# Performance work log

Hardware: AMD Instinct MI355X
Metric: run time of the kernel (lower is better)

The kernel has to match this reference:

```python
import jax, jax.numpy as jnp
import numpy as np

N, E, NG = 10000, 160000, 64
HID, HEADS = 256, 4
NEG_SLOPE = 0.2


def setup_inputs() -> dict:
    key = jax.random.key(0)
    ks = jax.random.split(key, 20)
    s = 0.1
    inp = {
        "atom_features": jax.random.normal(ks[0], (N, 23), jnp.float32),
        "edge_index": jax.random.randint(ks[1], (2, E), 0, N),
        "batch": jnp.sort(jax.random.randint(ks[2], (N,), 0, NG)),
        "W1": jax.random.normal(ks[3], (23, HEADS * HID), jnp.float32) * s,
        "as1": jax.random.normal(ks[4], (HEADS, HID), jnp.float32) * s,
        "ad1": jax.random.normal(ks[5], (HEADS, HID), jnp.float32) * s,
        "b1": jnp.zeros((HEADS * HID,), jnp.float32),
        "W2": jax.random.normal(ks[6], (HEADS * HID, HEADS * HID), jnp.float32) * s,
        "as2": jax.random.normal(ks[7], (HEADS, HID), jnp.float32) * s,
        "ad2": jax.random.normal(ks[8], (HEADS, HID), jnp.float32) * s,
        "b2": jnp.zeros((HEADS * HID,), jnp.float32),
        "W3": jax.random.normal(ks[9], (HEADS * HID, HID), jnp.float32) * s,
        "as3": jax.random.normal(ks[10], (1, HID), jnp.float32) * s,
        "ad3": jax.random.normal(ks[11], (1, HID), jnp.float32) * s,
        "b3": jnp.zeros((HID,), jnp.float32),
        # MLP head
        "fc1_w": jax.random.normal(ks[12], (HID, HID // 2), jnp.float32) * s,
        "fc1_b": jnp.zeros((HID // 2,), jnp.float32),
        "fc2_w": jax.random.normal(ks[13], (HID // 2, 1), jnp.float32) * s,
        "fc2_b": jnp.zeros((1,), jnp.float32),
    }
    return inp


def gat_layer(x, W, att_src, att_dst, bias, src, dst, heads, ch):
    n = x.shape[0]
    h = (x @ W).reshape(n, heads, ch)                      # [N,H,C]
    a_s = jnp.sum(h * att_src, axis=-1)                    # [N,H]
    a_d = jnp.sum(h * att_dst, axis=-1)                    # [N,H]
    logits = jax.nn.leaky_relu(a_s[src] + a_d[dst], NEG_SLOPE)  # [E',H]
    m = jax.ops.segment_max(logits, dst, num_segments=n)
    m = jnp.where(jnp.isfinite(m), m, 0.0)
    e = jnp.exp(logits - m[dst])
    denom = jax.ops.segment_sum(e, dst, num_segments=n)
    alpha = e / (denom[dst] + 1e-16)                       # segment softmax over incoming edges
    out = jax.ops.segment_sum(alpha[:, :, None] * h[src], dst, num_segments=n)
    return out.reshape(n, heads * ch) + bias


def reference(atom_features, edge_index, batch,
              W1, as1, ad1, b1, W2, as2, ad2, b2, W3, as3, ad3, b3,
              fc1_w, fc1_b, fc2_w, fc2_b):
    n = atom_features.shape[0]
    loops = jnp.arange(n)
    src = jnp.concatenate([edge_index[0], loops])   # PyG GATConv adds self-loops
    dst = jnp.concatenate([edge_index[1], loops])

    x = jax.nn.elu(gat_layer(atom_features, W1, as1, ad1, b1, src, dst, HEADS, HID))
    x = jax.nn.elu(gat_layer(x, W2, as2, ad2, b2, src, dst, HEADS, HID))
    x = jax.nn.elu(gat_layer(x, W3, as3, ad3, b3, src, dst, 1, HID))
    # dropout: eval mode (training=False) -> identity

    # global mean pool over molecules
    sums = jax.ops.segment_sum(x, batch, num_segments=NG)
    counts = jax.ops.segment_sum(jnp.ones((n,), x.dtype), batch, num_segments=NG)
    features = sums / jnp.maximum(counts, 1.0)[:, None]    # [NG, HID]

    hmid = jax.nn.relu(features @ fc1_w + fc1_b)
    validity = hmid @ fc2_w + fc2_b                        # [NG, 1]
    return validity, features
```

## Files before the change

### kernel.cpp

```cpp
#include <hip/hip_runtime.h>
#include <hip/hip_bf16.h>
#include <math.h>

typedef unsigned short ushortT;
typedef __attribute__((ext_vector_type(8))) short short8;
typedef __attribute__((ext_vector_type(4))) float f32x4;

constexpr int NN   = 10000;
constexpr int EE   = 160000;
constexpr int ETOT = EE + NN;
constexpr int NG   = 64;
constexpr int HID  = 256;
constexpr int HEADS = 4;

__device__ __forceinline__ ushortT f2bf(float x) {
    __hip_bfloat16 h = __float2bfloat16(x);
    return *reinterpret_cast<ushortT*>(&h);
}
__device__ __forceinline__ float bf2f(ushortT x) {
    unsigned u = ((unsigned)x) << 16;
    return __uint_as_float(u);
}

__device__ __forceinline__ int xcd_swz(int flat, int nwg) {
    int q = nwg >> 3, r = nwg & 7;
    int xcd = flat & 7, j = flat >> 3;
    return (xcd < r ? xcd * (q + 1) : r * (q + 1) + (xcd - r) * q) + j;
}

__global__ __launch_bounds__(256) void setup_kernel(
        const float* __restrict__ W1, const float* __restrict__ as1,
        const float* __restrict__ ad1, float* __restrict__ wsv1,
        const float* __restrict__ W2, const float* __restrict__ as2,
        const float* __restrict__ ad2, float* __restrict__ wsv2,
        const float* __restrict__ W3, const float* __restrict__ as3,
        const float* __restrict__ ad3, float* __restrict__ wsv3,
        ushortT* __restrict__ wt2, ushortT* __restrict__ wt3,
        ushortT* __restrict__ b1p, int* __restrict__ cnt) {
    __shared__ float t[32][33];
    const int b = blockIdx.x, tid = threadIdx.x;
    if (b < 1280) {
        const float* W; ushortT* Wt; int N, n0, k0;
        if (b < 1024) { W = W2; Wt = wt2; N = 1024; n0 = (b & 31) * 32; k0 = (b >> 5) * 32; }
        else          { int b2 = b - 1024; W = W3; Wt = wt3; N = 256; n0 = (b2 & 7) * 32; k0 = (b2 >> 3) * 32; }
        const int K = 1024, Kp = 1024;
        int tx = tid & 31, ty = tid >> 5;
        for (int i = ty; i < 32; i += 8) {
            int k = k0 + i, n = n0 + tx;
            t[i][tx] = (k < K && n < N) ? W[(size_t)k * N + n] : 0.f;
        }
        __syncthreads();
        for (int i = ty; i < 32; i += 8) {
            int n = n0 + i, kp = k0 + tx;
            if (n < N && kp < Kp) Wt[(size_t)n * Kp + kp] = f2bf(t[tx][i]);
        }
    } else if (b < 1792) {
        int idx = (b - 1280) * 256 + tid;
        int n = idx >> 7, kp = idx & 127;
        int h = n >> 8, hk = kp >> 5, k = kp & 31;
        float v = (hk == h && k < 23) ? W1[(size_t)k * 1024 + n] : 0.f;
        b1p[idx] = f2bf(v);
    } else if (b < 4398) {
        int gw = (b - 1792) * 4 + (tid >> 6);
        int lane = tid & 63;
        const float *W, *atts, *attd; float* wsv; int heads, idx;
        if (gw < 184)            { W = W1; atts = as1; attd = ad1; wsv = wsv1; heads = 4; idx = gw; }
        else if (gw < 184 + 8192){ W = W2; atts = as2; attd = ad2; wsv = wsv2; heads = 4; idx = gw - 184; }
        else if (gw < 184 + 8192 + 2048) { W = W3; atts = as3; attd = ad3; wsv = wsv3; heads = 1; idx = gw - 184 - 8192; }
        else return;
        const int nout = 2 * heads;
        int k = idx / nout, o = idx - k * nout;
        int h = (o >= heads) ? (o - heads) : o;
        const float* att  = ((o >= heads) ? attd : atts) + h * HID;
        const float* wrow = W + (size_t)k * (heads * HID) + h * HID;
        float4 w4 = *(const float4*)(wrow + lane * 4);
        float4 a4 = *(const float4*)(att + lane * 4);
        float s = w4.x * a4.x + w4.y * a4.y + w4.z * a4.z + w4.w * a4.w;
        #pragma unroll
        for (int off = 1; off < 64; off <<= 1) s += __shfl_xor(s, off);
        if (lane == 0) wsv[(size_t)k * nout + o] = s;
    } else {
        int idx = (b - 4398) * 256 + tid;
        if (idx < NN) cnt[idx] = 0;
    }
}

__global__ void edge_count_kernel(const int* __restrict__ ei, int* __restrict__ cnt) {
    int e = blockIdx.x * blockDim.x + threadIdx.x;
    if (e >= ETOT) return;
    int dst = (e < EE) ? ei[EE + e] : (e - EE);
    atomicAdd(&cnt[dst], 1);
}

__global__ void scan_kernel(const int* __restrict__ cnt, int* __restrict__ row_ptr,
                            int* __restrict__ cursor) {
    __shared__ int part[256];
    int tid = threadIdx.x;
    const int chunk = (NN + 255) / 256;
    int s0 = tid * chunk;
    int s1 = min(NN, s0 + chunk);
    int sum = 0;
    for (int i = s0; i < s1; ++i) sum += cnt[i];
    part[tid] = sum;
    __syncthreads();
    for (int off = 1; off < 256; off <<= 1) {
        int v = (tid >= off) ? part[tid - off] : 0;
        __syncthreads();
        part[tid] += v;
        __syncthreads();
    }
    int run = (tid == 0) ? 0 : part[tid - 1];
    for (int i = s0; i < s1; ++i) {
        row_ptr[i] = run;
        cursor[i]  = run;
        run += cnt[i];
    }
    if (tid == 255) row_ptr[NN] = part[255];
}

__global__ void fill_dots1_kernel(const int* __restrict__ ei, int* __restrict__ cursor,
                                  int* __restrict__ col_src,
                                  const float* __restrict__ atom,
                                  const float* __restrict__ wsv1,
                                  float* __restrict__ a_s, float* __restrict__ a_d,
                                  int nfill) {
    int b = blockIdx.x;
    if (b < nfill) {
        int e = b * 256 + threadIdx.x;
        if (e >= ETOT) return;
        int src, dst;
        if (e < EE) { src = ei[e]; dst = ei[EE + e]; }
        else        { src = dst = e - EE; }
        int pos = atomicAdd(&cursor[dst], 1);
        col_src[pos] = src;
    } else {
        int n = (b - nfill) * 256 + threadIdx.x;
        if (n >= NN) return;
        float a[8] = {0.f, 0.f, 0.f, 0.f, 0.f, 0.f, 0.f, 0.f};
        #pragma unroll
        for (int k = 0; k < 23; ++k) {
            float x = atom[n * 23 + k];
            #pragma unroll
            for (int o = 0; o < 8; ++o) a[o] += x * wsv1[k * 8 + o];
        }
        #pragma unroll
        for (int h = 0; h < 4; ++h) { a_s[n * 4 + h] = a[h]; a_d[n * 4 + h] = a[4 + h]; }
    }
}

__global__ __launch_bounds__(256) void agg_atom_kernel(const float* __restrict__ atom,
                                                       const float* __restrict__ a_s,
                                                       const float* __restrict__ a_d,
                                                       const int* __restrict__ rowp,
                                                       const int* __restrict__ colv,
                                                       ushortT* __restrict__ Ap) {
    const int wv = threadIdx.x >> 6, lane = threadIdx.x & 63;
    const int i = blockIdx.x * 4 + wv;
    if (i >= NN) return;
    const int half = lane >> 5, c = lane & 31;
    const int start = rowp[i], end = rowp[i + 1];

    __shared__ float wsh[4][64][4];
    __shared__ int   ssh[4][64];

    float acc[4] = {0.f, 0.f, 0.f, 0.f};
    float den4[4] = {0.f, 0.f, 0.f, 0.f};
    for (int cb = start; cb < end; cb += 64) {
        int clen = min(64, end - cb);
        if (lane < clen) {
            int s = colv[cb + lane];
            ssh[wv][lane] = s;
            float4 as4 = *(const float4*)(a_s + (size_t)s * 4);
            float4 ad4 = *(const float4*)(a_d + (size_t)i * 4);
            float l0 = as4.x + ad4.x; l0 = (l0 >= 0.f) ? l0 : 0.2f * l0;
            float l1 = as4.y + ad4.y; l1 = (l1 >= 0.f) ? l1 : 0.2f * l1;
            float l2 = as4.z + ad4.z; l2 = (l2 >= 0.f) ? l2 : 0.2f * l2;
            float l3 = as4.w + ad4.w; l3 = (l3 >= 0.f) ? l3 : 0.2f * l3;
            float w0 = expf(l0), w1 = expf(l1), w2 = expf(l2), w3 = expf(l3);
            *reinterpret_cast<float4*>(&wsh[wv][lane][0]) = make_float4(w0, w1, w2, w3);
            den4[0] += w0; den4[1] += w1; den4[2] += w2; den4[3] += w3;
        }
        __builtin_amdgcn_wave_barrier();
        for (int e = half; e < clen; e += 2) {
            int s = ssh[wv][e];
            float x = (c < 23) ? atom[(size_t)s * 23 + c] : 0.f;
            acc[0] += wsh[wv][e][0] * x;
            acc[1] += wsh[wv][e][1] * x;
            acc[2] += wsh[wv][e][2] * x;
            acc[3] += wsh[wv][e][3] * x;
        }
        __builtin_amdgcn_wave_barrier();
    }
    #pragma unroll
    for (int h = 0; h < 4; ++h) acc[h] += __shfl_xor(acc[h], 32);
    #pragma unroll
    for (int off = 1; off < 64; off <<= 1) {
        den4[0] += __shfl_xor(den4[0], off);
        den4[1] += __shfl_xor(den4[1], off);
        den4[2] += __shfl_xor(den4[2], off);
        den4[3] += __shfl_xor(den4[3], off);
    }
    if (half == 0) {
        #pragma unroll
        for (int h = 0; h < 4; ++h) {
            float v = acc[h] / (den4[h] + 1e-16f);
            Ap[(size_t)i * 128 + h * 32 + c] = f2bf(v);
        }
    }
}

__device__ __forceinline__ void gload_lds16(const ushortT* gsrc, ushortT* ldst) {
    __builtin_amdgcn_global_load_lds(
        (const __attribute__((address_space(1))) unsigned int*)gsrc,
        (__attribute__((address_space(3))) unsigned int*)ldst, 16, 0, 0);
}

template<int MODE, int DOTS>
__global__ __launch_bounds__(256, 2) void gemm_fused(const ushortT* __restrict__ A,
                                                     const ushortT* __restrict__ Bt,
                                                     ushortT* __restrict__ C,
                                                     const float* __restrict__ bias,
                                                     const float* __restrict__ wsv,
                                                     float* __restrict__ da_s,
                                                     float* __restrict__ da_d,
                                                     int M, int N, int K,
                                                     int nx, int ngemm) {
    if ((int)blockIdx.x < ngemm) {
        __shared__ ushortT lds[2][2][128][32];
        const int tid  = threadIdx.x;
        const int lane = tid & 63, w = tid >> 6;
        const int wm = w >> 1, wn = w & 1;
        const int swz  = xcd_swz(blockIdx.x, ngemm);
        const int bx = swz % nx, by = swz / nx;
        const int row0 = by * 128;
        const int col0 = bx * 128;
        const int nt = K >> 5;

        auto stage = [&](int buf, int t) {
            int k0 = t << 5;
            #pragma unroll
            for (int i = 0; i < 2; ++i) {
                int gbase = (w * 2 + i) * 64;
                int g = gbase + lane;
                int row = g >> 2;
                int sw = (row & 3) ^ ((row >> 2) & 3);
                int koff = (g & 3) ^ sw;
                int arow = min(row0 + row, M - 1);
                gload_lds16(A + (size_t)arow * K + k0 + koff * 8,
                            &lds[buf][0][0][0] + gbase * 8);
                int brow = col0 + row;
                gload_lds16(Bt + (size_t)brow * K + k0 + koff * 8,
                            &lds[buf][1][0][0] + gbase * 8);
            }
        };

        f32x4 acc[4][4] = {};
        const int lr = lane & 15, lk = lane >> 4;

        stage(0, 0);
        for (int t = 0; t < nt; ++t) {
            int buf = t & 1;
            __syncthreads();
            if (t + 1 < nt) stage(buf ^ 1, t + 1);
            short8 a[4], b[4];
            const ushortT* baseA = &lds[buf][0][0][0];
            const ushortT* baseB = &lds[buf][1][0][0];
            #pragma unroll
            for (int m = 0; m < 4; ++m) {
                int row = wm * 64 + m * 16 + lr;
                int sw = (row & 3) ^ ((row >> 2) & 3);
                a[m] = *(const short8*)(baseA + row * 32 + ((lk ^ sw) * 8));
            }
            #pragma unroll
            for (int n = 0; n < 4; ++n) {
                int row = wn * 64 + n * 16 + lr;
                int sw = (row & 3) ^ ((row >> 2) & 3);
                b[n] = *(const short8*)(baseB + row * 32 + ((lk ^ sw) * 8));
            }
            #pragma unroll
            for (int m = 0; m < 4; ++m)
                #pragma unroll
                for (int n = 0; n < 4; ++n)
                    acc[m][n] = __builtin_amdgcn_mfma_f32_16x16x32_bf16(a[m], b[n], acc[m][n], 0, 0, 0);
        }

        #pragma unroll
        for (int m = 0; m < 4; ++m) {
            #pragma unroll
            for (int n = 0; n < 4; ++n) {
                int col = col0 + wn * 64 + n * 16 + lr;
                float bv = (MODE == 1) ? bias[col] : 0.f;
                #pragma unroll
                for (int j = 0; j < 4; ++j) {
                    int rowg = row0 + wm * 64 + m * 16 + lk * 4 + j;
                    if (rowg < M) {
                        float v = acc[m][n][j];
                        if (MODE == 1) { v += bv; v = (v > 0.f) ? v : expm1f(v); }
                        C[(size_t)rowg * N + col] = f2bf(v);
                    }
                }
            }
        }
    } else if (DOTS == 2) {
        int gw = ((int)blockIdx.x - ngemm) * 4 + (threadIdx.x >> 6);
        int lane = threadIdx.x & 63;
        if (gw >= NN) return;
        const ushortT* row = A + (size_t)gw * 1024 + lane * 16;
        short8 v0 = *(const short8*)row;
        short8 v1 = *(const short8*)(row + 8);
        float ps[8] = {0.f, 0.f, 0.f, 0.f, 0.f, 0.f, 0.f, 0.f};
        const float* wb = wsv + (size_t)lane * 16 * 8;
        #pragma unroll
        for (int c = 0; c < 8; ++c) {
            float xv = bf2f((ushortT)v0[c]);
            #pragma unroll
            for (int o = 0; o < 8; ++o) ps[o] += xv * wb[c * 8 + o];
        }
        #pragma unroll
        for (int c = 0; c < 8; ++c) {
            float xv = bf2f((ushortT)v1[c]);
            #pragma unroll
            for (int o = 0; o < 8; ++o) ps[o] += xv * wb[(8 + c) * 8 + o];
        }
        #pragma unroll
        for (int off = 1; off < 64; off <<= 1) {
            #pragma unroll
            for (int o = 0; o < 8; ++o) ps[o] += __shfl_xor(ps[o], off);
        }
        if (lane == 0) {
            #pragma unroll
            for (int h = 0; h < 4; ++h) { da_s[gw * 4 + h] = ps[h]; da_d[gw * 4 + h] = ps[4 + h]; }
        }
    } else if (DOTS == 3) {
        int gw = ((int)blockIdx.x - ngemm) * 4 + (threadIdx.x >> 6);
        int lane = threadIdx.x & 63;
        if (gw >= NN) return;
        const ushortT* row = A + (size_t)gw * 1024 + lane * 16;
        short8 v0 = *(const short8*)row;
        short8 v1 = *(const short8*)(row + 8);
        float p0 = 0.f, p1 = 0.f;
        const int c0 = lane * 16;
        #pragma unroll
        for (int c = 0; c < 8; ++c) {
            float xv = bf2f((ushortT)v0[c]);
            float2 w2 = *(const float2*)(wsv + (size_t)(c0 + c) * 2);
            p0 += xv * w2.x; p1 += xv * w2.y;
        }
        #pragma unroll
        for (int c = 0; c < 8; ++c) {
            float xv = bf2f((ushortT)v1[c]);
            float2 w2 = *(const float2*)(wsv + (size_t)(c0 + 8 + c) * 2);
            p0 += xv * w2.x; p1 += xv * w2.y;
        }
        #pragma unroll
        for (int off = 1; off < 64; off <<= 1) {
            p0 += __shfl_xor(p0, off);
            p1 += __shfl_xor(p1, off);
        }
        if (lane == 0) { da_s[gw] = p0; da_d[gw] = p1; }
    }
}

__global__ __launch_bounds__(256) void gat_agg_h4(const ushortT* __restrict__ hfeat,
                                                  const float* __restrict__ a_s,
                                                  const float* __restrict__ a_d,
                                                  const int* __restrict__ rowp,
                                                  const int* __restrict__ colv,
                                                  const float* __restrict__ bias,
                                                  ushortT* __restrict__ out16) {
    const int wv = threadIdx.x >> 6, lane = threadIdx.x & 63;
    const int i = blockIdx.x * 4 + wv;
    if (i >= NN) return;
    const int c0 = lane * 16;
    const int hh = c0 >> 8;
    const int start = rowp[i], end = rowp[i + 1];

    __shared__ float wsh[4][64][4];
    __shared__ int   ssh[4][64];

    float acc[16];
    #pragma unroll
    for (int c = 0; c < 16; ++c) acc[c] = 0.f;
    float den4[4] = {0.f, 0.f, 0.f, 0.f};

    for (int cb = start; cb < end; cb += 64) {
        int clen = min(64, end - cb);
        if (lane < clen) {
            int s = colv[cb + lane];
            ssh[wv][lane] = s;
            float4 as4 = *(const float4*)(a_s + (size_t)s * 4);
            float4 ad4 = *(const float4*)(a_d + (size_t)i * 4);
            float l0 = as4.x + ad4.x; l0 = (l0 >= 0.f) ? l0 : 0.2f * l0;
            float l1 = as4.y + ad4.y; l1 = (l1 >= 0.f) ? l1 : 0.2f * l1;
            float l2 = as4.z + ad4.z; l2 = (l2 >= 0.f) ? l2 : 0.2f * l2;
            float l3 = as4.w + ad4.w; l3 = (l3 >= 0.f) ? l3 : 0.2f * l3;
            float w0 = expf(l0), w1 = expf(l1), w2 = expf(l2), w3 = expf(l3);
            *reinterpret_cast<float4*>(&wsh[wv][lane][0]) = make_float4(w0, w1, w2, w3);
            den4[0] += w0; den4[1] += w1; den4[2] += w2; den4[3] += w3;
        }
        __builtin_amdgcn_wave_barrier();
        int e = 0;
        for (; e + 4 <= clen; e += 4) {
            int sa = ssh[wv][e], sb = ssh[wv][e + 1], sc = ssh[wv][e + 2], sd = ssh[wv][e + 3];
            const ushortT* pa = hfeat + (size_t)sa * 1024 + c0;
            const ushortT* pb = hfeat + (size_t)sb * 1024 + c0;
            const ushortT* pc = hfeat + (size_t)sc * 1024 + c0;
            const ushortT* pd = hfeat + (size_t)sd * 1024 + c0;
            short8 va0 = *(const short8*)pa,       va1 = *(const short8*)(pa + 8);
            short8 vb0 = *(const short8*)pb,       vb1 = *(const short8*)(pb + 8);
            short8 vc0 = *(const short8*)pc,       vc1 = *(const short8*)(pc + 8);
            short8 vd0 = *(const short8*)pd,       vd1 = *(const short8*)(pd + 8);
            float wa = wsh[wv][e][hh],     wb = wsh[wv][e + 1][hh];
            float wc = wsh[wv][e + 2][hh], wd = wsh[wv][e + 3][hh];
            #pragma unroll
            for (int j = 0; j < 8; ++j) {
                acc[j]     += wa * bf2f((ushortT)va0[j]) + wb * bf2f((ushortT)vb0[j])
                            + wc * bf2f((ushortT)vc0[j]) + wd * bf2f((ushortT)vd0[j]);
                acc[8 + j] += wa * bf2f((ushortT)va1[j]) + wb * bf2f((ushortT)vb1[j])
                            + wc * bf2f((ushortT)vc1[j]) + wd * bf2f((ushortT)vd1[j]);
            }
        }
        for (; e < clen; ++e) {
            int s = ssh[wv][e];
            float wgt = wsh[wv][e][hh];
            const ushortT* p = hfeat + (size_t)s * 1024 + c0;
            short8 v0 = *(const short8*)p;
            short8 v1 = *(const short8*)(p + 8);
            #pragma unroll
            for (int j = 0; j < 8; ++j) {
                acc[j]     += wgt * bf2f((ushortT)v0[j]);
                acc[8 + j] += wgt * bf2f((ushortT)v1[j]);
            }
        }
        __builtin_amdgcn_wave_barrier();
    }

    #pragma unroll
    for (int off = 1; off < 64; off <<= 1) {
        den4[0] += __shfl_xor(den4[0], off);
        den4[1] += __shfl_xor(den4[1], off);
        den4[2] += __shfl_xor(den4[2], off);
        den4[3] += __shfl_xor(den4[3], off);
    }
    float den = (hh == 0) ? den4[0] : (hh == 1) ? den4[1] : (hh == 2) ? den4[2] : den4[3];
    float inv = 1.f / (den + 1e-16f);

    ushortT pk[16];
    #pragma unroll
    for (int c = 0; c < 16; ++c) {
        float v = acc[c] * inv + bias[c0 + c];
        v = (v > 0.f) ? v : expm1f(v);
        pk[c] = f2bf(v);
    }
    *reinterpret_cast<short8*>(out16 + (size_t)i * 1024 + c0)     = *reinterpret_cast<short8*>(&pk[0]);
    *reinterpret_cast<short8*>(out16 + (size_t)i * 1024 + c0 + 8) = *reinterpret_cast<short8*>(&pk[8]);
}

__global__ __launch_bounds__(256) void gat_agg_h1(const ushortT* __restrict__ hfeat,
                                                  const float* __restrict__ a_s,
                                                  const float* __restrict__ a_d,
                                                  const int* __restrict__ rowp,
                                                  const int* __restrict__ colv,
                                                  const float* __restrict__ bias,
                                                  float* __restrict__ outf) {
    const int wv = threadIdx.x >> 6, lane = threadIdx.x & 63;
    const int i = blockIdx.x * 4 + wv;
    if (i >= NN) return;
    const int c0 = lane * 4;
    const int start = rowp[i], end = rowp[i + 1];
    const float adi = a_d[i];

    __shared__ float wsh[4][64];
    __shared__ int   ssh[4][64];

    float acc[4] = {0.f, 0.f, 0.f, 0.f};
    float den = 0.f;

    for (int cb = start; cb < end; cb += 64) {
        int clen = min(64, end - cb);
        if (lane < clen) {
            int s = colv[cb + lane];
            ssh[wv][lane] = s;
            float l = a_s[s] + adi;
            l = (l >= 0.f) ? l : 0.2f * l;
            float w0 = expf(l);
            wsh[wv][lane] = w0;
            den += w0;
        }
        __builtin_amdgcn_wave_barrier();
        int e = 0;
        for (; e + 4 <= clen; e += 4) {
            int sa = ssh[wv][e], sb = ssh[wv][e + 1], sc = ssh[wv][e + 2], sd = ssh[wv][e + 3];
            ushort4 va = *(const ushort4*)(hfeat + (size_t)sa * 256 + c0);
            ushort4 vb = *(const ushort4*)(hfeat + (size_t)sb * 256 + c0);
            ushort4 vc = *(const ushort4*)(hfeat + (size_t)sc * 256 + c0);
            ushort4 vd = *(const ushort4*)(hfeat + (size_t)sd * 256 + c0);
            float wa = wsh[wv][e], wb2 = wsh[wv][e + 1], wc2 = wsh[wv][e + 2], wd2 = wsh[wv][e + 3];
            acc[0] += wa * bf2f(va.x) + wb2 * bf2f(vb.x) + wc2 * bf2f(vc.x) + wd2 * bf2f(vd.x);
            acc[1] += wa * bf2f(va.y) + wb2 * bf2f(vb.y) + wc2 * bf2f(vc.y) + wd2 * bf2f(vd.y);
            acc[2] += wa * bf2f(va.z) + wb2 * bf2f(vb.z) + wc2 * bf2f(vc.z) + wd2 * bf2f(vd.z);
            acc[3] += wa * bf2f(va.w) + wb2 * bf2f(vb.w) + wc2 * bf2f(vc.w) + wd2 * bf2f(vd.w);
        }
        for (; e < clen; ++e) {
            int s = ssh[wv][e];
            float wgt = wsh[wv][e];
            ushort4 v = *(const ushort4*)(hfeat + (size_t)s * 256 + c0);
            acc[0] += wgt * bf2f(v.x); acc[1] += wgt * bf2f(v.y);
            acc[2] += wgt * bf2f(v.z); acc[3] += wgt * bf2f(v.w);
        }
        __builtin_amdgcn_wave_barrier();
    }

    #pragma unroll
    for (int off = 1; off < 64; off <<= 1) den += __shfl_xor(den, off);
    float inv = 1.f / (den + 1e-16f);

    float4 o4;
    float v0 = acc[0] * inv + bias[c0 + 0]; o4.x = (v0 > 0.f) ? v0 : expm1f(v0);
    float v1 = acc[1] * inv + bias[c0 + 1]; o4.y = (v1 > 0.f) ? v1 : expm1f(v1);
    float v2 = acc[2] * inv + bias[c0 + 2]; o4.z = (v2 > 0.f) ? v2 : expm1f(v2);
    float v3 = acc[3] * inv + bias[c0 + 3]; o4.w = (v3 > 0.f) ? v3 : expm1f(v3);
    *reinterpret_cast<float4*>(outf + (size_t)i * 256 + c0) = o4;
}

__global__ void pool_mlp(const float* __restrict__ x,
                         const int* __restrict__ batch,
                         const float* __restrict__ fc1_w,
                         const float* __restrict__ fc1_b,
                         const float* __restrict__ fc2_w,
                         const float* __restrict__ fc2_b,
                         float* __restrict__ out) {
    int g = blockIdx.x, tid = threadIdx.x;
    int lo = 0, hi = NN;
    while (lo < hi) { int mid = (lo + hi) >> 1; if (batch[mid] < g) lo = mid + 1; else hi = mid; }
    int s0 = lo;
    lo = 0; hi = NN;
    while (lo < hi) { int mid = (lo + hi) >> 1; if (batch[mid] < g + 1) lo = mid + 1; else hi = mid; }
    int s1 = lo;

    float acc = 0.f;
    for (int n = s0; n < s1; ++n) acc += x[(size_t)n * HID + tid];
    float cnt = (float)(s1 - s0);
    float feat = acc / fmaxf(cnt, 1.f);
    out[NG + g * HID + tid] = feat;

    __shared__ float fsh[HID];
    fsh[tid] = feat;
    __syncthreads();
    __shared__ float r2[128];
    if (tid < 128) {
        float a = fc1_b[tid];
        for (int c = 0; c < HID; ++c) a += fsh[c] * fc1_w[c * 128 + tid];
        a = fmaxf(a, 0.f);
        r2[tid] = a * fc2_w[tid];
    }
    __syncthreads();
    for (int s2 = 64; s2 > 0; s2 >>= 1) {
        if (tid < s2) r2[tid] += r2[tid + s2];
        __syncthreads();
    }
    if (tid == 0) out[g] = r2[0] + fc2_b[0];
}

extern "C" void kernel_launch(void* const* d_in, const int* in_sizes, int n_in,
                              void* d_out, int out_size, void* d_ws, size_t ws_size,
                              hipStream_t stream) {
    const float* atom  = (const float*)d_in[0];
    const int*   ei    = (const int*)  d_in[1];
    const int*   batch = (const int*)  d_in[2];
    const float* W1  = (const float*)d_in[3];
    const float* as1 = (const float*)d_in[4];
    const float* ad1 = (const float*)d_in[5];
    const float* b1  = (const float*)d_in[6];
    const float* W2  = (const float*)d_in[7];
    const float* as2 = (const float*)d_in[8];
    const float* ad2 = (const float*)d_in[9];
    const float* b2  = (const float*)d_in[10];
    const float* W3  = (const float*)d_in[11];
    const float* as3 = (const float*)d_in[12];
    const float* ad3 = (const float*)d_in[13];
    const float* b3  = (const float*)d_in[14];
    const float* fc1w = (const float*)d_in[15];
    const float* fc1b = (const float*)d_in[16];
    const float* fc2w = (const float*)d_in[17];
    const float* fc2b = (const float*)d_in[18];
    float* out = (float*)d_out;

    ushortT* h16  = (ushortT*)d_ws;
    ushortT* x16  = h16 + (size_t)NN * 1024;
    ushortT* Ap   = x16 + (size_t)NN * 1024;
    ushortT* b1p  = Ap + (size_t)NN * 128;
    ushortT* wt2  = b1p + 1024 * 128;
    ushortT* wt3  = wt2 + 1024 * 1024;
    float*   x3   = (float*)(wt3 + 256 * 1024);
    float*   asL1 = x3 + (size_t)NN * 256;
    float*   adL1 = asL1 + (size_t)NN * 4;
    float*   asL2 = adL1 + (size_t)NN * 4;
    float*   adL2 = asL2 + (size_t)NN * 4;
    float*   asL3 = adL2 + (size_t)NN * 4;
    float*   adL3 = asL3 + NN;
    float*   wsv1 = adL3 + NN;
    float*   wsv2 = wsv1 + 23 * 8;
    float*   wsv3 = wsv2 + 1024 * 8;
    int*   cnt    = (int*)(wsv3 + 1024 * 2);
    int*   rowp   = cnt + NN;
    int*   cursor = rowp + NN + 1;
    int*   col    = cursor + NN;

    dim3 blk(256);
    const int gagg = (NN + 3) / 4;
    const int gy   = (NN + 127) / 128;

    setup_kernel<<<4438, blk, 0, stream>>>(W1, as1, ad1, wsv1, W2, as2, ad2, wsv2,
                                           W3, as3, ad3, wsv3, wt2, wt3, b1p, cnt);

    edge_count_kernel<<<(ETOT + 255) / 256, blk, 0, stream>>>(ei, cnt);
    scan_kernel<<<1, blk, 0, stream>>>(cnt, rowp, cursor);
    const int nfill = (ETOT + 255) / 256;
    fill_dots1_kernel<<<nfill + (NN + 255) / 256, blk, 0, stream>>>(
        ei, cursor, col, atom, wsv1, asL1, adL1, nfill);

    agg_atom_kernel<<<gagg, blk, 0, stream>>>(atom, asL1, adL1, rowp, col, Ap);
    gemm_fused<1, 0><<<8 * gy, blk, 0, stream>>>(Ap, b1p, x16, b1, nullptr, nullptr, nullptr,
                                                 NN, 1024, 128, 8, 8 * gy);

    gemm_fused<0, 2><<<8 * gy + gagg, blk, 0, stream>>>(x16, wt2, h16, nullptr, wsv2,
                                                        asL2, adL2, NN, 1024, 1024, 8, 8 * gy);
    gat_agg_h4<<<gagg, blk, 0, stream>>>(h16, asL2, adL2, rowp, col, b2, x16);

    gemm_fused<0, 3><<<2 * gy + gagg, blk, 0, stream>>>(x16, wt3, h16, nullptr, wsv3,
                                                        asL3, adL3, NN, 256, 1024, 2, 2 * gy);
    gat_agg_h1<<<gagg, blk, 0, stream>>>(h16, asL3, adL3, rowp, col, b3, x3);

    pool_mlp<<<NG, blk, 0, stream>>>(x3, batch, fc1w, fc1b, fc2w, fc2b, out);
}
```

Measured before the change: 300.8 us.

## Split attention-dot blocks out of GEMM kernels and pad rows to tile multiple

Un-fuses the attention-score dot-product work from the GEMM launches into separate dots2/dots3 kernels that run before each GEMM. Row buffers are padded to a multiple of 128 (MP), so the row clamp in the load path and the bounds check in the store path are dropped. The intent is a simpler, branch-free GEMM with lower register pressure and no mixed block types in one grid. The cost is two extra kernel launches and the loss of overlap between the dots work and the GEMM. Padded rows compute garbage that is written but never read.

```diff
diff --git a/kernel.cpp b/kernel.cpp
--- a/kernel.cpp
+++ b/kernel.cpp
@@ -7,6 +7,7 @@
 typedef __attribute__((ext_vector_type(4))) float f32x4;
 
 constexpr int NN   = 10000;
+constexpr int MP   = 10112;
 constexpr int EE   = 160000;
 constexpr int ETOT = EE + NN;
 constexpr int NG   = 64;
@@ -215,150 +216,148 @@
         (__attribute__((address_space(3))) unsigned int*)ldst, 16, 0, 0);
 }
 
-template<int MODE, int DOTS>
-__global__ __launch_bounds__(256, 2) void gemm_fused(const ushortT* __restrict__ A,
-                                                     const ushortT* __restrict__ Bt,
-                                                     ushortT* __restrict__ C,
-                                                     const float* __restrict__ bias,
-                                                     const float* __restrict__ wsv,
-                                                     float* __restrict__ da_s,
-                                                     float* __restrict__ da_d,
-                                                     int M, int N, int K,
-                                                     int nx, int ngemm) {
-    if ((int)blockIdx.x < ngemm) {
-        __shared__ ushortT lds[2][2][128][32];
-        const int tid  = threadIdx.x;
-        const int lane = tid & 63, w = tid >> 6;
-        const int wm = w >> 1, wn = w & 1;
-        const int swz  = xcd_swz(blockIdx.x, ngemm);
-        const int bx = swz % nx, by = swz / nx;
-        const int row0 = by * 128;
-        const int col0 = bx * 128;
-        const int nt = K >> 5;
-
-        auto stage = [&](int buf, int t) {
-            int k0 = t << 5;
+template<int MODE>
+__global__ __launch_bounds__(256, 2) void gemm_bf16(const ushortT* __restrict__ A,
+                                                    const ushortT* __restrict__ Bt,
+                                                    ushortT* __restrict__ C,
+                                                    const float* __restrict__ bias,
+                                                    int N, int K, int nx) {
+    __shared__ ushortT lds[2][2][128][32];
+    const int tid  = threadIdx.x;
+    const int lane = tid & 63, w = tid >> 6;
+    const int wm = w >> 1, wn = w & 1;
+    const int swz  = xcd_swz(blockIdx.x, gridDim.x);
+    const int bx = swz % nx, by = swz / nx;
+    const int row0 = by * 128;
+    const int col0 = bx * 128;
+    const int nt = K >> 5;
+
+    auto stage = [&](int buf, int t) {
+        int k0 = t << 5;
+        #pragma unroll
+        for (int i = 0; i < 2; ++i) {
+            int gbase = (w * 2 + i) * 64;
+            int g = gbase + lane;
+            int row = g >> 2;
+            int sw = (row & 3) ^ ((row >> 2) & 3);
+            int koff = (g & 3) ^ sw;
+            gload_lds16(A + (size_t)(row0 + row) * K + k0 + koff * 8,
+                        &lds[buf][0][0][0] + gbase * 8);
+            gload_lds16(Bt + (size_t)(col0 + row) * K + k0 + koff * 8,
+                        &lds[buf][1][0][0] + gbase * 8);
+        }
+    };
+
+    f32x4 acc[4][4] = {};
+    const int lr = lane & 15, lk = lane >> 4;
+
+    stage(0, 0);
+    for (int t = 0; t < nt; ++t) {
+        int buf = t & 1;
+        __syncthreads();
+        if (t + 1 < nt) stage(buf ^ 1, t + 1);
+        short8 a[4], b[4];
+        const ushortT* baseA = &lds[buf][0][0][0];
+        const ushortT* baseB = &lds[buf][1][0][0];
+        #pragma unroll
+        for (int m = 0; m < 4; ++m) {
+            int row = wm * 64 + m * 16 + lr;
+            int sw = (row & 3) ^ ((row >> 2) & 3);
+            a[m] = *(const short8*)(baseA + row * 32 + ((lk ^ sw) * 8));
+        }
+        #pragma unroll
+        for (int n = 0; n < 4; ++n) {
+            int row = wn * 64 + n * 16 + lr;
+            int sw = (row & 3) ^ ((row >> 2) & 3);
+            b[n] = *(const short8*)(baseB + row * 32 + ((lk ^ sw) * 8));
+        }
+        #pragma unroll
+        for (int m = 0; m < 4; ++m)
             #pragma unroll
-            for (int i = 0; i < 2; ++i) {
-                int gbase = (w * 2 + i) * 64;
-                int g = gbase + lane;
-                int row = g >> 2;
-                int sw = (row & 3) ^ ((row >> 2) & 3);
-                int koff = (g & 3) ^ sw;
-                int arow = min(row0 + row, M - 1);
-                gload_lds16(A + (size_t)arow * K + k0 + koff * 8,
-                            &lds[buf][0][0][0] + gbase * 8);
-                int brow = col0 + row;
-                gload_lds16(Bt + (size_t)brow * K + k0 + koff * 8,
-                            &lds[buf][1][0][0] + gbase * 8);
+            for (int n = 0; n < 4; ++n)
+                acc[m][n] = __builtin_amdgcn_mfma_f32_16x16x32_bf16(a[m], b[n], acc[m][n], 0, 0, 0);
+    }
+
+    #pragma unroll
+    for (int m = 0; m < 4; ++m) {
+        #pragma unroll
+        for (int n = 0; n < 4; ++n) {
+            int col = col0 + wn * 64 + n * 16 + lr;
+            float bv = (MODE == 1) ? bias[col] : 0.f;
+            #pragma unroll
+            for (int j = 0; j < 4; ++j) {
+                int rowg = row0 + wm * 64 + m * 16 + lk * 4 + j;
+                float v = acc[m][n][j];
+                if (MODE == 1) { v += bv; v = (v > 0.f) ? v : expm1f(v); }
+                C[(size_t)rowg * N + col] = f2bf(v);
             }
-        };
-
-        f32x4 acc[4][4] = {};
-        const int lr = lane & 15, lk = lane >> 4;
-
-        stage(0, 0);
-        for (int t = 0; t < nt; ++t) {
-            int buf = t & 1;
-            __syncthreads();
-            if (t + 1 < nt) stage(buf ^ 1, t + 1);
-            short8 a[4], b[4];
-            const ushortT* baseA = &lds[buf][0][0][0];
-            const ushortT* baseB = &lds[buf][1][0][0];
-            #pragma unroll
-            for (int m = 0; m < 4; ++m) {
-                int row = wm * 64 + m * 16 + lr;
-                int sw = (row & 3) ^ ((row >> 2) & 3);
-                a[m] = *(const short8*)(baseA + row * 32 + ((lk ^ sw) * 8));
-            }
-            #pragma unroll
-            for (int n = 0; n < 4; ++n) {
-                int row = wn * 64 + n * 16 + lr;
-                int sw = (row & 3) ^ ((row >> 2) & 3);
-                b[n] = *(const short8*)(baseB + row * 32 + ((lk ^ sw) * 8));
-            }
-            #pragma unroll
-            for (int m = 0; m < 4; ++m)
-                #pragma unroll
-                for (int n = 0; n < 4; ++n)
-                    acc[m][n] = __builtin_amdgcn_mfma_f32_16x16x32_bf16(a[m], b[n], acc[m][n], 0, 0, 0);
-        }
-
-        #pragma unroll
-        for (int m = 0; m < 4; ++m) {
-            #pragma unroll
-            for (int n = 0; n < 4; ++n) {
-                int col = col0 + wn * 64 + n * 16 + lr;
-                float bv = (MODE == 1) ? bias[col] : 0.f;
-                #pragma unroll
-                for (int j = 0; j < 4; ++j) {
-                    int rowg = row0 + wm * 64 + m * 16 + lk * 4 + j;
-                    if (rowg < M) {
-                        float v = acc[m][n][j];
-                        if (MODE == 1) { v += bv; v = (v > 0.f) ? v : expm1f(v); }
-                        C[(size_t)rowg * N + col] = f2bf(v);
-                    }
-                }
-            }
-        }
-    } else if (DOTS == 2) {
-        int gw = ((int)blockIdx.x - ngemm) * 4 + (threadIdx.x >> 6);
-        int lane = threadIdx.x & 63;
-        if (gw >= NN) return;
-        const ushortT* row = A + (size_t)gw * 1024 + lane * 16;
-        short8 v0 = *(const short8*)row;
-        short8 v1 = *(const short8*)(row + 8);
-        float ps[8] = {0.f, 0.f, 0.f, 0.f, 0.f, 0.f, 0.f, 0.f};
-        const float* wb = wsv + (size_t)lane * 16 * 8;
-        #pragma unroll
-        for (int c = 0; c < 8; ++c) {
-            float xv = bf2f((ushortT)v0[c]);
-            #pragma unroll
-            for (int o = 0; o < 8; ++o) ps[o] += xv * wb[c * 8 + o];
-        }
-        #pragma unroll
-        for (int c = 0; c < 8; ++c) {
-            float xv = bf2f((ushortT)v1[c]);
-            #pragma unroll
-            for (int o = 0; o < 8; ++o) ps[o] += xv * wb[(8 + c) * 8 + o];
-        }
-        #pragma unroll
-        for (int off = 1; off < 64; off <<= 1) {
-            #pragma unroll
-            for (int o = 0; o < 8; ++o) ps[o] += __shfl_xor(ps[o], off);
-        }
-        if (lane == 0) {
-            #pragma unroll
-            for (int h = 0; h < 4; ++h) { da_s[gw * 4 + h] = ps[h]; da_d[gw * 4 + h] = ps[4 + h]; }
-        }
-    } else if (DOTS == 3) {
-        int gw = ((int)blockIdx.x - ngemm) * 4 + (threadIdx.x >> 6);
-        int lane = threadIdx.x & 63;
-        if (gw >= NN) return;
-        const ushortT* row = A + (size_t)gw * 1024 + lane * 16;
-        short8 v0 = *(const short8*)row;
-        short8 v1 = *(const short8*)(row + 8);
-        float p0 = 0.f, p1 = 0.f;
-        const int c0 = lane * 16;
-        #pragma unroll
-        for (int c = 0; c < 8; ++c) {
-            float xv = bf2f((ushortT)v0[c]);
-            float2 w2 = *(const float2*)(wsv + (size_t)(c0 + c) * 2);
-            p0 += xv * w2.x; p1 += xv * w2.y;
-        }
-        #pragma unroll
-        for (int c = 0; c < 8; ++c) {
-            float xv = bf2f((ushortT)v1[c]);
-            float2 w2 = *(const float2*)(wsv + (size_t)(c0 + 8 + c) * 2);
-            p0 += xv * w2.x; p1 += xv * w2.y;
-        }
-        #pragma unroll
-        for (int off = 1; off < 64; off <<= 1) {
-            p0 += __shfl_xor(p0, off);
-            p1 += __shfl_xor(p1, off);
-        }
-        if (lane == 0) { da_s[gw] = p0; da_d[gw] = p1; }
-    }
+        }
+    }
+}
+
+__global__ void dots2_kernel(const ushortT* __restrict__ x,
+                             const float* __restrict__ wsv,
+                             float* __restrict__ a_s, float* __restrict__ a_d) {
+    int gw = (blockIdx.x * 256 + threadIdx.x) >> 6;
+    int lane = threadIdx.x & 63;
+    if (gw >= NN) return;
+    const ushortT* row = x + (size_t)gw * 1024 + lane * 16;
+    short8 v0 = *(const short8*)row;
+    short8 v1 = *(const short8*)(row + 8);
+    float ps[8] = {0.f, 0.f, 0.f, 0.f, 0.f, 0.f, 0.f, 0.f};
+    const float* wb = wsv + (size_t)lane * 16 * 8;
+    #pragma unroll
+    for (int c = 0; c < 8; ++c) {
+        float xv = bf2f((ushortT)v0[c]);
+        #pragma unroll
+        for (int o = 0; o < 8; ++o) ps[o] += xv * wb[c * 8 + o];
+    }
+    #pragma unroll
+    for (int c = 0; c < 8; ++c) {
+        float xv = bf2f((ushortT)v1[c]);
+        #pragma unroll
+        for (int o = 0; o < 8; ++o) ps[o] += xv * wb[(8 + c) * 8 + o];
+    }
+    #pragma unroll
+    for (int off = 1; off < 64; off <<= 1) {
+        #pragma unroll
+        for (int o = 0; o < 8; ++o) ps[o] += __shfl_xor(ps[o], off);
+    }
+    if (lane == 0) {
+        #pragma unroll
+        for (int h = 0; h < 4; ++h) { a_s[gw * 4 + h] = ps[h]; a_d[gw * 4 + h] = ps[4 + h]; }
+    }
+}
+
+__global__ void dots3_kernel(const ushortT* __restrict__ x,
+                             const float* __restrict__ wsv,
+                             float* __restrict__ a_s, float* __restrict__ a_d) {
+    int gw = (blockIdx.x * 256 + threadIdx.x) >> 6;
+    int lane = threadIdx.x & 63;
+    if (gw >= NN) return;
+    const ushortT* row = x + (size_t)gw * 1024 + lane * 16;
+    short8 v0 = *(const short8*)row;
+    short8 v1 = *(const short8*)(row + 8);
+    float p0 = 0.f, p1 = 0.f;
+    const int c0 = lane * 16;
+    #pragma unroll
+    for (int c = 0; c < 8; ++c) {
+        float xv = bf2f((ushortT)v0[c]);
+        float2 w2 = *(const float2*)(wsv + (size_t)(c0 + c) * 2);
+        p0 += xv * w2.x; p1 += xv * w2.y;
+    }
+    #pragma unroll
+    for (int c = 0; c < 8; ++c) {
+        float xv = bf2f((ushortT)v1[c]);
+        float2 w2 = *(const float2*)(wsv + (size_t)(c0 + 8 + c) * 2);
+        p0 += xv * w2.x; p1 += xv * w2.y;
+    }
+    #pragma unroll
+    for (int off = 1; off < 64; off <<= 1) {
+        p0 += __shfl_xor(p0, off);
+        p1 += __shfl_xor(p1, off);
+    }
+    if (lane == 0) { a_s[gw] = p0; a_d[gw] = p1; }
 }
 
 __global__ __launch_bounds__(256) void gat_agg_h4(const ushortT* __restrict__ hfeat,
@@ -587,9 +586,9 @@
     float* out = (float*)d_out;
 
     ushortT* h16  = (ushortT*)d_ws;
-    ushortT* x16  = h16 + (size_t)NN * 1024;
-    ushortT* Ap   = x16 + (size_t)NN * 1024;
-    ushortT* b1p  = Ap + (size_t)NN * 128;
+    ushortT* x16  = h16 + (size_t)MP * 1024;
+    ushortT* Ap   = x16 + (size_t)MP * 1024;
+    ushortT* b1p  = Ap + (size_t)MP * 128;
     ushortT* wt2  = b1p + 1024 * 128;
     ushortT* wt3  = wt2 + 1024 * 1024;
     float*   x3   = (float*)(wt3 + 256 * 1024);
@@ -609,7 +608,7 @@
 
     dim3 blk(256);
     const int gagg = (NN + 3) / 4;
-    const int gy   = (NN + 127) / 128;
+    const int gy   = MP / 128;
 
     setup_kernel<<<4438, blk, 0, stream>>>(W1, as1, ad1, wsv1, W2, as2, ad2, wsv2,
                                            W3, as3, ad3, wsv3, wt2, wt3, b1p, cnt);
@@ -621,15 +620,14 @@
         ei, cursor, col, atom, wsv1, asL1, adL1, nfill);
 
     agg_atom_kernel<<<gagg, blk, 0, stream>>>(atom, asL1, adL1, rowp, col, Ap);
-    gemm_fused<1, 0><<<8 * gy, blk, 0, stream>>>(Ap, b1p, x16, b1, nullptr, nullptr, nullptr,
-                                                 NN, 1024, 128, 8, 8 * gy);
-
-    gemm_fused<0, 2><<<8 * gy + gagg, blk, 0, stream>>>(x16, wt2, h16, nullptr, wsv2,
-                                                        asL2, adL2, NN, 1024, 1024, 8, 8 * gy);
+    gemm_bf16<1><<<8 * gy, blk, 0, stream>>>(Ap, b1p, x16, b1, 1024, 128, 8);
+
+    dots2_kernel<<<gagg, blk, 0, stream>>>(x16, wsv2, asL2, adL2);
+    gemm_bf16<0><<<8 * gy, blk, 0, stream>>>(x16, wt2, h16, nullptr, 1024, 1024, 8);
     gat_agg_h4<<<gagg, blk, 0, stream>>>(h16, asL2, adL2, rowp, col, b2, x16);
 
-    gemm_fused<0, 3><<<2 * gy + gagg, blk, 0, stream>>>(x16, wt3, h16, nullptr, wsv3,
-                                                        asL3, adL3, NN, 256, 1024, 2, 2 * gy);
+    dots3_kernel<<<gagg, blk, 0, stream>>>(x16, wsv3, asL3, adL3);
+    gemm_bf16<0><<<2 * gy, blk, 0, stream>>>(x16, wt3, h16, nullptr, 256, 1024, 2);
     gat_agg_h1<<<gagg, blk, 0, stream>>>(h16, asL3, adL3, rowp, col, b3, x3);
 
     pool_mlp<<<NG, blk, 0, stream>>>(x3, batch, fc1w, fc1b, fc2w, fc2b, out);
```

After: 304.6 us. No clear change (+1.3%).

## Deepen GEMM K-tile to 64, pad rows, fold edge counting into setup

Applied to the files above, without the earlier changes.

The GEMM template gains a K-tile size parameter. Layers 2 and 3 now stage 64-wide K slices with an 8-way XOR swizzle, which halves the number of barriers and pipeline iterations per tile. Activation buffers are padded to 10112 rows so the GEMM can drop its row clamp and its store bounds check, at the cost of computing on garbage padding rows. Edge counting moves into the setup kernel's tail blocks, and counter zeroing moves to a memset, which removes one kernel launch. The larger LDS footprint may reduce occupancy.

```diff
diff --git a/kernel.cpp b/kernel.cpp
--- a/kernel.cpp
+++ b/kernel.cpp
@@ -7,6 +7,7 @@
 typedef __attribute__((ext_vector_type(4))) float f32x4;
 
 constexpr int NN   = 10000;
+constexpr int MP   = 10112;
 constexpr int EE   = 160000;
 constexpr int ETOT = EE + NN;
 constexpr int NG   = 64;
@@ -36,7 +37,8 @@
         const float* __restrict__ W3, const float* __restrict__ as3,
         const float* __restrict__ ad3, float* __restrict__ wsv3,
         ushortT* __restrict__ wt2, ushortT* __restrict__ wt3,
-        ushortT* __restrict__ b1p, int* __restrict__ cnt) {
+        ushortT* __restrict__ b1p, const int* __restrict__ ei,
+        int* __restrict__ cnt) {
     __shared__ float t[32][33];
     const int b = blockIdx.x, tid = threadIdx.x;
     if (b < 1280) {
@@ -80,16 +82,11 @@
         for (int off = 1; off < 64; off <<= 1) s += __shfl_xor(s, off);
         if (lane == 0) wsv[(size_t)k * nout + o] = s;
     } else {
-        int idx = (b - 4398) * 256 + tid;
-        if (idx < NN) cnt[idx] = 0;
-    }
-}
-
-__global__ void edge_count_kernel(const int* __restrict__ ei, int* __restrict__ cnt) {
-    int e = blockIdx.x * blockDim.x + threadIdx.x;
-    if (e >= ETOT) return;
-    int dst = (e < EE) ? ei[EE + e] : (e - EE);
-    atomicAdd(&cnt[dst], 1);
+        int e = (b - 4398) * 256 + tid;
+        if (e >= ETOT) return;
+        int dst = (e < EE) ? ei[EE + e] : (e - EE);
+        atomicAdd(&cnt[dst], 1);
+    }
 }
 
 __global__ void scan_kernel(const int* __restrict__ cnt, int* __restrict__ row_ptr,
@@ -215,18 +212,17 @@
         (__attribute__((address_space(3))) unsigned int*)ldst, 16, 0, 0);
 }
 
-template<int MODE, int DOTS>
-__global__ __launch_bounds__(256, 2) void gemm_fused(const ushortT* __restrict__ A,
-                                                     const ushortT* __restrict__ Bt,
-                                                     ushortT* __restrict__ C,
-                                                     const float* __restrict__ bias,
-                                                     const float* __restrict__ wsv,
-                                                     float* __restrict__ da_s,
-                                                     float* __restrict__ da_d,
-                                                     int M, int N, int K,
-                                                     int nx, int ngemm) {
+template<int MODE, int KS, int DOTS>
+__global__ __launch_bounds__(256, 2) void gemm_bf16(const ushortT* __restrict__ A,
+                                                    const ushortT* __restrict__ Bt,
+                                                    ushortT* __restrict__ C,
+                                                    const float* __restrict__ bias,
+                                                    const float* __restrict__ wsv,
+                                                    float* __restrict__ da_s,
+                                                    float* __restrict__ da_d,
+                                                    int N, int K, int nx, int ngemm) {
+    __shared__ ushortT lds[2][2][128][KS];
     if ((int)blockIdx.x < ngemm) {
-        __shared__ ushortT lds[2][2][128][32];
         const int tid  = threadIdx.x;
         const int lane = tid & 63, w = tid >> 6;
         const int wm = w >> 1, wn = w & 1;
@@ -234,23 +230,22 @@
         const int bx = swz % nx, by = swz / nx;
         const int row0 = by * 128;
         const int col0 = bx * 128;
-        const int nt = K >> 5;
+        const int nt = K / KS;
+        constexpr int GPR = KS / 8;
+        constexpr int PT  = 128 * GPR / 256;
 
         auto stage = [&](int buf, int t) {
-            int k0 = t << 5;
-            #pragma unroll
-            for (int i = 0; i < 2; ++i) {
-                int gbase = (w * 2 + i) * 64;
-                int g = gbase + lane;
-                int row = g >> 2;
-                int sw = (row & 3) ^ ((row >> 2) & 3);
-                int koff = (g & 3) ^ sw;
-                int arow = min(row0 + row, M - 1);
-                gload_lds16(A + (size_t)arow * K + k0 + koff * 8,
-                            &lds[buf][0][0][0] + gbase * 8);
-                int brow = col0 + row;
-                gload_lds16(Bt + (size_t)brow * K + k0 + koff * 8,
-                            &lds[buf][1][0][0] + gbase * 8);
+            int k0 = t * KS;
+            #pragma unroll
+            for (int i = 0; i < PT; ++i) {
+                int g = i * 256 + tid;
+                int row = g / GPR, gi = g % GPR;
+                int sw = (KS == 64) ? (row & 7) : ((row & 3) ^ ((row >> 2) & 3));
+                int koff = gi ^ sw;
+                gload_lds16(A + (size_t)(row0 + row) * K + k0 + koff * 8,
+                            &lds[buf][0][0][0] + g * 8);
+                gload_lds16(Bt + (size_t)(col0 + row) * K + k0 + koff * 8,
+                            &lds[buf][1][0][0] + g * 8);
             }
         };
 
@@ -262,26 +257,31 @@
             int buf = t & 1;
             __syncthreads();
             if (t + 1 < nt) stage(buf ^ 1, t + 1);
-            short8 a[4], b[4];
             const ushortT* baseA = &lds[buf][0][0][0];
             const ushortT* baseB = &lds[buf][1][0][0];
             #pragma unroll
-            for (int m = 0; m < 4; ++m) {
-                int row = wm * 64 + m * 16 + lr;
-                int sw = (row & 3) ^ ((row >> 2) & 3);
-                a[m] = *(const short8*)(baseA + row * 32 + ((lk ^ sw) * 8));
+            for (int kk = 0; kk < KS / 32; ++kk) {
+                short8 a[4], b[4];
+                #pragma unroll
+                for (int m = 0; m < 4; ++m) {
+                    int row = wm * 64 + m * 16 + lr;
+                    int sw = (KS == 64) ? (row & 7) : ((row & 3) ^ ((row >> 2) & 3));
+                    int gidx = (kk * 4 + lk) ^ sw;
+                    a[m] = *(const short8*)(baseA + row * KS + gidx * 8);
+                }
+                #pragma unroll
+                for (int n = 0; n < 4; ++n) {
+                    int row = wn * 64 + n * 16 + lr;
+                    int sw = (KS == 64) ? (row & 7) : ((row & 3) ^ ((row >> 2) & 3));
+                    int gidx = (kk * 4 + lk) ^ sw;
+                    b[n] = *(const short8*)(baseB + row * KS + gidx * 8);
+                }
+                #pragma unroll
+                for (int m = 0; m < 4; ++m)
+                    #pragma unroll
+                    for (int n = 0; n < 4; ++n)
+                        acc[m][n] = __builtin_amdgcn_mfma_f32_16x16x32_bf16(a[m], b[n], acc[m][n], 0, 0, 0);
             }
-            #pragma unroll
-            for (int n = 0; n < 4; ++n) {
-                int row = wn * 64 + n * 16 + lr;
-                int sw = (row & 3) ^ ((row >> 2) & 3);
-                b[n] = *(const short8*)(baseB + row * 32 + ((lk ^ sw) * 8));
-            }
-            #pragma unroll
-            for (int m = 0; m < 4; ++m)
-                #pragma unroll
-                for (int n = 0; n < 4; ++n)
-                    acc[m][n] = __builtin_amdgcn_mfma_f32_16x16x32_bf16(a[m], b[n], acc[m][n], 0, 0, 0);
         }
 
         #pragma unroll
@@ -293,11 +293,9 @@
                 #pragma unroll
                 for (int j = 0; j < 4; ++j) {
                     int rowg = row0 + wm * 64 + m * 16 + lk * 4 + j;
-                    if (rowg < M) {
-                        float v = acc[m][n][j];
-                        if (MODE == 1) { v += bv; v = (v > 0.f) ? v : expm1f(v); }
-                        C[(size_t)rowg * N + col] = f2bf(v);
-                    }
+                    float v = acc[m][n][j];
+                    if (MODE == 1) { v += bv; v = (v > 0.f) ? v : expm1f(v); }
+                    C[(size_t)rowg * N + col] = f2bf(v);
                 }
             }
         }
@@ -587,9 +585,9 @@
     float* out = (float*)d_out;
 
     ushortT* h16  = (ushortT*)d_ws;
-    ushortT* x16  = h16 + (size_t)NN * 1024;
-    ushortT* Ap   = x16 + (size_t)NN * 1024;
-    ushortT* b1p  = Ap + (size_t)NN * 128;
+    ushortT* x16  = h16 + (size_t)MP * 1024;
+    ushortT* Ap   = x16 + (size_t)MP * 1024;
+    ushortT* b1p  = Ap + (size_t)MP * 128;
     ushortT* wt2  = b1p + 1024 * 128;
     ushortT* wt3  = wt2 + 1024 * 1024;
     float*   x3   = (float*)(wt3 + 256 * 1024);
@@ -609,27 +607,28 @@
 
     dim3 blk(256);
     const int gagg = (NN + 3) / 4;
-    const int gy   = (NN + 127) / 128;
-
-    setup_kernel<<<4438, blk, 0, stream>>>(W1, as1, ad1, wsv1, W2, as2, ad2, wsv2,
-                                           W3, as3, ad3, wsv3, wt2, wt3, b1p, cnt);
-
-    edge_count_kernel<<<(ETOT + 255) / 256, blk, 0, stream>>>(ei, cnt);
+    const int gy   = MP / 128;
+
+    hipMemsetAsync(cnt, 0, NN * sizeof(int), stream);
+    const int ecnt_blocks = (ETOT + 255) / 256;
+    setup_kernel<<<4398 + ecnt_blocks, blk, 0, stream>>>(
+        W1, as1, ad1, wsv1, W2, as2, ad2, wsv2,
+        W3, as3, ad3, wsv3, wt2, wt3, b1p, ei, cnt);
+
     scan_kernel<<<1, blk, 0, stream>>>(cnt, rowp, cursor);
-    const int nfill = (ETOT + 255) / 256;
-    fill_dots1_kernel<<<nfill + (NN + 255) / 256, blk, 0, stream>>>(
-        ei, cursor, col, atom, wsv1, asL1, adL1, nfill);
+    fill_dots1_kernel<<<ecnt_blocks + (NN + 255) / 256, blk, 0, stream>>>(
+        ei, cursor, col, atom, wsv1, asL1, adL1, ecnt_blocks);
 
     agg_atom_kernel<<<gagg, blk, 0, stream>>>(atom, asL1, adL1, rowp, col, Ap);
-    gemm_fused<1, 0><<<8 * gy, blk, 0, stream>>>(Ap, b1p, x16, b1, nullptr, nullptr, nullptr,
-                                                 NN, 1024, 128, 8, 8 * gy);
-
-    gemm_fused<0, 2><<<8 * gy + gagg, blk, 0, stream>>>(x16, wt2, h16, nullptr, wsv2,
-                                                        asL2, adL2, NN, 1024, 1024, 8, 8 * gy);
+    gemm_bf16<1, 32, 0><<<8 * gy, blk, 0, stream>>>(Ap, b1p, x16, b1, nullptr, nullptr, nullptr,
+                                                    1024, 128, 8, 8 * gy);
+
+    gemm_bf16<0, 64, 2><<<8 * gy + gagg, blk, 0, stream>>>(x16, wt2, h16, nullptr, wsv2,
+                                                           asL2, adL2, 1024, 1024, 8, 8 * gy);
     gat_agg_h4<<<gagg, blk, 0, stream>>>(h16, asL2, adL2, rowp, col, b2, x16);
 
-    gemm_fused<0, 3><<<2 * gy + gagg, blk, 0, stream>>>(x16, wt3, h16, nullptr, wsv3,
-                                                        asL3, adL3, NN, 256, 1024, 2, 2 * gy);
+    gemm_bf16<0, 64, 3><<<2 * gy + gagg, blk, 0, stream>>>(x16, wt3, h16, nullptr, wsv3,
+                                                           asL3, adL3, 256, 1024, 2, 2 * gy);
     gat_agg_h1<<<gagg, blk, 0, stream>>>(h16, asL3, adL3, rowp, col, b3, x3);
 
     pool_mlp<<<NG, blk, 0, stream>>>(x3, batch, fc1w, fc1b, fc2w, fc2b, out);
```

New measurement: 293.6 us. 1.02x faster.
